# Kernel optimization log

Hardware: AMD Instinct MI355X
Metric: run time of the kernel (lower is better)

Reference implementation:

```python
import jax, jax.numpy as jnp
import numpy as np

B, L, E, H = 8, 1024, 1024, 16
D = E // H
EPS = 1e-5


def setup_inputs() -> dict:
    key = jax.random.key(0)
    ks = jax.random.split(key, 3)
    s = 1.0 / np.sqrt(E)
    return {
        "x": jax.random.normal(ks[0], (B, L, E), dtype=jnp.float32),
        "w_qkv": jax.random.normal(ks[1], (3 * E, E), dtype=jnp.float32) * s,
        "b_qkv": jnp.zeros((3 * E,), dtype=jnp.float32),
        "w_out": jax.random.normal(ks[2], (E, E), dtype=jnp.float32) * s,
        "b_out": jnp.zeros((E,), dtype=jnp.float32),
        "gamma": jnp.ones((E,), dtype=jnp.float32),
        "beta": jnp.zeros((E,), dtype=jnp.float32),
    }


def reference(x, w_qkv, b_qkv, w_out, b_out, gamma, beta):
    # Packed QKV projection (torch nn.MultiheadAttention in_proj): (B,L,3E)
    qkv = jnp.einsum("ble,fe->blf", x, w_qkv) + b_qkv
    q, k, v = jnp.split(qkv, 3, axis=-1)
    # (B,L,H,D)
    q = q.reshape(B, L, H, D) * (1.0 / np.sqrt(D))
    k = k.reshape(B, L, H, D)
    v = v.reshape(B, L, H, D)
    scores = jnp.einsum("blhd,bmhd->bhlm", q, k)           # (B,H,L,L)
    w = jax.nn.softmax(scores, axis=-1)                     # (B,H,L,L)
    ctx = jnp.einsum("bhlm,bmhd->blhd", w, v).reshape(B, L, E)
    attn_out = jnp.einsum("ble,fe->blf", ctx, w_out) + b_out
    # Residual + LayerNorm
    h = x + attn_out
    mu = h.mean(axis=-1, keepdims=True)
    var = ((h - mu) ** 2).mean(axis=-1, keepdims=True)
    hn = (h - mu) * jax.lax.rsqrt(var + EPS) * gamma + beta
    pooled = hn.mean(axis=1)                                # (B,E)
    # torch returns head-averaged weights (B,L,L); then mean over query dim
    avg_attn = w.mean(axis=1).mean(axis=1)                  # (B,L)
    return pooled, avg_attn
```

## Files before the change

### kernel.cpp

```cpp
#include <hip/hip_runtime.h>
#include <math.h>

constexpr int Bc = 8;
constexpr int Lc = 1024;
constexpr int Ec = 1024;
constexpr int Hc = 16;
constexpr int Dc = 64;
constexpr float EPSc = 1e-5f;

typedef _Float16 f16;
typedef f16 half8 __attribute__((ext_vector_type(8)));
typedef float floatx4 __attribute__((ext_vector_type(4)));

static __device__ inline void gload_lds16(const f16* g, f16* l) {
    __builtin_amdgcn_global_load_lds(
        (const __attribute__((address_space(1))) void*)g,
        (__attribute__((address_space(3))) void*)l, 16, 0, 0);
}

__global__ __launch_bounds__(256)
void cvt_f32_f16_kernel(const float* __restrict__ src, f16* __restrict__ dst, int n8) {
    int i = blockIdx.x * 256 + threadIdx.x;
    const int stride = gridDim.x * 256;
    for (; i < n8; i += stride) {
        float4 a = *(const float4*)(src + (size_t)i * 8);
        float4 b = *(const float4*)(src + (size_t)i * 8 + 4);
        half8 p;
        p[0] = (f16)a.x; p[1] = (f16)a.y; p[2] = (f16)a.z; p[3] = (f16)a.w;
        p[4] = (f16)b.x; p[5] = (f16)b.y; p[6] = (f16)b.z; p[7] = (f16)b.w;
        *(half8*)(dst + (size_t)i * 8) = p;
    }
}

__global__ __launch_bounds__(256)
void gemm_nt_h(const f16* __restrict__ A, const f16* __restrict__ Bm,
               const float* __restrict__ bias, float* __restrict__ Cf,
               f16* __restrict__ Ch, int M, int N, int K) {
    constexpr int TILE = 128;
    constexpr int KT = 32;
    __shared__ __align__(16) f16 As[TILE * KT];
    __shared__ __align__(16) f16 Bs[TILE * KT];

    const int tid = threadIdx.x;
    const int bm = blockIdx.x * TILE;
    const int bn = blockIdx.y * TILE;

    const int wave = tid >> 6;
    const int lane = tid & 63;
    const int wm = (wave >> 1) * 64;
    const int wn = (wave & 1) * 64;
    const int r16 = lane & 15;
    const int kg = lane >> 4;
    const int kswz = kg ^ ((r16 >> 1) & 3);

    floatx4 acc[4][4];
#pragma unroll
    for (int i = 0; i < 4; ++i)
#pragma unroll
        for (int j = 0; j < 4; ++j) acc[i][j] = (floatx4){0.f, 0.f, 0.f, 0.f};

    const int c0 = tid, c1 = 256 + tid;
    const int row0 = c0 >> 2, row1 = c1 >> 2;
    const int kc0 = (c0 & 3) ^ ((row0 >> 1) & 3);
    const int kc1 = (c1 & 3) ^ ((row1 >> 1) & 3);
    const f16* a0p = A + (size_t)(bm + row0) * K + kc0 * 8;
    const f16* a1p = A + (size_t)(bm + row1) * K + kc1 * 8;
    const f16* b0p = Bm + (size_t)(bn + row0) * K + kc0 * 8;
    const f16* b1p = Bm + (size_t)(bn + row1) * K + kc1 * 8;
    f16* asl0 = As + c0 * 8;
    f16* asl1 = As + c1 * 8;
    f16* bsl0 = Bs + c0 * 8;
    f16* bsl1 = Bs + c1 * 8;

    for (int k0 = 0; k0 < K; k0 += KT) {
        __syncthreads();
        gload_lds16(a0p + k0, asl0);
        gload_lds16(a1p + k0, asl1);
        gload_lds16(b0p + k0, bsl0);
        gload_lds16(b1p + k0, bsl1);
        __syncthreads();

        half8 af[4], bf[4];
#pragma unroll
        for (int i = 0; i < 4; ++i)
            af[i] = *(const half8*)&As[(wm + 16 * i + r16) * KT + kswz * 8];
#pragma unroll
        for (int j = 0; j < 4; ++j)
            bf[j] = *(const half8*)&Bs[(wn + 16 * j + r16) * KT + kswz * 8];
#pragma unroll
        for (int i = 0; i < 4; ++i)
#pragma unroll
            for (int j = 0; j < 4; ++j)
                acc[i][j] = __builtin_amdgcn_mfma_f32_16x16x32_f16(af[i], bf[j], acc[i][j], 0, 0, 0);
    }

    if (Ch) {
#pragma unroll
        for (int j = 0; j < 4; ++j) {
            const int col = bn + wn + 16 * j + r16;
            const float bv = bias[col];
#pragma unroll
            for (int i = 0; i < 4; ++i) {
                const int row0e = bm + wm + 16 * i + kg * 4;
#pragma unroll
                for (int r = 0; r < 4; ++r)
                    Ch[(size_t)(row0e + r) * N + col] = (f16)(acc[i][j][r] + bv);
            }
        }
    } else {
#pragma unroll
        for (int j = 0; j < 4; ++j) {
            const int col = bn + wn + 16 * j + r16;
            const float bv = bias[col];
#pragma unroll
            for (int i = 0; i < 4; ++i) {
                const int row0e = bm + wm + 16 * i + kg * 4;
#pragma unroll
                for (int r = 0; r < 4; ++r)
                    Cf[(size_t)(row0e + r) * N + col] = acc[i][j][r] + bv;
            }
        }
    }
}

constexpr int AQT = 128;
constexpr int AKT = 128;
constexpr int AKP = 72;
constexpr int AWP = 136;
constexpr int AVP = 136;

constexpr int AQ_OFF  = 0;
constexpr int AKV_OFF = 4608;
constexpr int AW_OFF  = AKV_OFF + 4608;
constexpr int ARS_OFF = AW_OFF + 8704;
constexpr int ACOL_OFF = ARS_OFF + 128;
constexpr int ASMEM   = ACOL_OFF + 1024;

__global__ __launch_bounds__(256, 2)
void attn_kernel(const f16* __restrict__ qkv, f16* __restrict__ ctx,
                 float* __restrict__ avg_out) {
    __shared__ __align__(16) float smemf[ASMEM];
    f16* Kq = (f16*)(smemf + AQ_OFF);
    f16* Kt = (f16*)(smemf + AKV_OFF);
    f16* Vt = (f16*)(smemf + AKV_OFF);
    f16* WS = (f16*)(smemf + AW_OFF);
    float* RS  = smemf + ARS_OFF;
    float* COL = smemf + ACOL_OFF;

    const int tid = threadIdx.x;
    const int qt = blockIdx.x, h = blockIdx.y, b = blockIdx.z;
    const int l0 = qt * AQT;
    const size_t rowstride = 3 * Ec;
    const f16* base = qkv + (size_t)b * Lc * rowstride + (size_t)h * Dc;

    const int wave = tid >> 6, lane = tid & 63;
    const int r16 = lane & 15, kg = lane >> 4;
    const int wm = (wave >> 1) * 64;
    const int wn = (wave & 1) * 64;

    if (tid < 128) RS[tid] = 0.f;
#pragma unroll
    for (int t = 0; t < 4; ++t) COL[t * 256 + tid] = 0.f;

    const int srow = tid >> 1;
    const int sh = (tid & 1) * 32;

    {
        const f16* src = base + (size_t)(l0 + srow) * rowstride + sh;
        f16* dst = Kq + srow * AKP + sh;
#pragma unroll
        for (int jj = 0; jj < 4; ++jj) {
            half8 p = *(const half8*)(src + jj * 8);
#pragma unroll
            for (int e = 0; e < 8; ++e) p[e] = p[e] * (f16)0.125f;
            *(half8*)(dst + jj * 8) = p;
        }
    }

    float rs[4][4];
#pragma unroll
    for (int i = 0; i < 4; ++i)
#pragma unroll
        for (int r = 0; r < 4; ++r) rs[i][r] = 0.f;

    for (int kt = 0; kt < Lc / AKT; ++kt) {
        __syncthreads();
        {
            const f16* src = base + (size_t)(kt * AKT + srow) * rowstride + Ec + sh;
            f16* dst = Kt + srow * AKP + sh;
#pragma unroll
            for (int jj = 0; jj < 4; ++jj)
                *(half8*)(dst + jj * 8) = *(const half8*)(src + jj * 8);
        }
        __syncthreads();

        floatx4 s[4][4];
#pragma unroll
        for (int i = 0; i < 4; ++i)
#pragma unroll
            for (int j = 0; j < 4; ++j) s[i][j] = (floatx4){0.f, 0.f, 0.f, 0.f};
#pragma unroll
        for (int ks = 0; ks < 2; ++ks) {
            half8 af[4], bf[4];
#pragma unroll
            for (int i = 0; i < 4; ++i)
                af[i] = *(const half8*)&Kq[(wm + 16 * i + r16) * AKP + ks * 32 + kg * 8];
#pragma unroll
            for (int j = 0; j < 4; ++j)
                bf[j] = *(const half8*)&Kt[(wn + 16 * j + r16) * AKP + ks * 32 + kg * 8];
#pragma unroll
            for (int i = 0; i < 4; ++i)
#pragma unroll
                for (int j = 0; j < 4; ++j)
                    s[i][j] = __builtin_amdgcn_mfma_f32_16x16x32_f16(af[i], bf[j], s[i][j], 0, 0, 0);
        }
#pragma unroll
        for (int i = 0; i < 4; ++i)
#pragma unroll
            for (int r = 0; r < 4; ++r)
                rs[i][r] += __expf(s[i][0][r]) + __expf(s[i][1][r]) +
                            __expf(s[i][2][r]) + __expf(s[i][3][r]);
    }

#pragma unroll
    for (int i = 0; i < 4; ++i)
#pragma unroll
        for (int r = 0; r < 4; ++r) {
            float v = rs[i][r];
            v += __shfl_xor(v, 1); v += __shfl_xor(v, 2);
            v += __shfl_xor(v, 4); v += __shfl_xor(v, 8);
            rs[i][r] = v;
        }
    if (r16 == 0) {
#pragma unroll
        for (int i = 0; i < 4; ++i)
#pragma unroll
            for (int r = 0; r < 4; ++r)
                atomicAdd(&RS[wm + 16 * i + 4 * kg + r], rs[i][r]);
    }
    __syncthreads();
    if (tid < 128) RS[tid] = 1.0f / RS[tid];
    __syncthreads();

    float rinv[4][4];
#pragma unroll
    for (int i = 0; i < 4; ++i)
#pragma unroll
        for (int r = 0; r < 4; ++r) rinv[i][r] = RS[wm + 16 * i + 4 * kg + r];

    floatx4 cacc[2][4];
#pragma unroll
    for (int p = 0; p < 2; ++p)
#pragma unroll
        for (int j = 0; j < 4; ++j) cacc[p][j] = (floatx4){0.f, 0.f, 0.f, 0.f};
    const int qb = wave * 32;

    for (int kt = 0; kt < Lc / AKT; ++kt) {
        __syncthreads();
        {
            const f16* src = base + (size_t)(kt * AKT + srow) * rowstride + Ec + sh;
            f16* dst = Kt + srow * AKP + sh;
#pragma unroll
            for (int jj = 0; jj < 4; ++jj)
                *(half8*)(dst + jj * 8) = *(const half8*)(src + jj * 8);
        }
        __syncthreads();

        floatx4 s[4][4];
#pragma unroll
        for (int i = 0; i < 4; ++i)
#pragma unroll
            for (int j = 0; j < 4; ++j) s[i][j] = (floatx4){0.f, 0.f, 0.f, 0.f};
#pragma unroll
        for (int ks = 0; ks < 2; ++ks) {
            half8 af[4], bf[4];
#pragma unroll
            for (int i = 0; i < 4; ++i)
                af[i] = *(const half8*)&Kq[(wm + 16 * i + r16) * AKP + ks * 32 + kg * 8];
#pragma unroll
            for (int j = 0; j < 4; ++j)
                bf[j] = *(const half8*)&Kt[(wn + 16 * j + r16) * AKP + ks * 32 + kg * 8];
#pragma unroll
            for (int i = 0; i < 4; ++i)
#pragma unroll
                for (int j = 0; j < 4; ++j)
                    s[i][j] = __builtin_amdgcn_mfma_f32_16x16x32_f16(af[i], bf[j], s[i][j], 0, 0, 0);
        }

        float cs[4] = {0.f, 0.f, 0.f, 0.f};
#pragma unroll
        for (int i = 0; i < 4; ++i)
#pragma unroll
            for (int j = 0; j < 4; ++j)
#pragma unroll
                for (int r = 0; r < 4; ++r) {
                    float w = __expf(s[i][j][r]) * rinv[i][r];
                    s[i][j][r] = w;
                    cs[j] += w;
                }

        __syncthreads();

#pragma unroll
        for (int i = 0; i < 4; ++i)
#pragma unroll
            for (int r = 0; r < 4; ++r) {
                f16* wrow = WS + (wm + 16 * i + 4 * kg + r) * AWP + wn + r16;
#pragma unroll
                for (int j = 0; j < 4; ++j) wrow[16 * j] = (f16)s[i][j][r];
            }

        {
            const f16* src = base + (size_t)(kt * AKT + srow) * rowstride + 2 * Ec + sh;
#pragma unroll
            for (int jj = 0; jj < 4; ++jj) {
                half8 v = *(const half8*)(src + jj * 8);
#pragma unroll
                for (int e = 0; e < 8; ++e)
                    Vt[(sh + jj * 8 + e) * AVP + srow] = v[e];
            }
        }

#pragma unroll
        for (int j = 0; j < 4; ++j) {
            float c = cs[j];
            c += __shfl_xor(c, 16);
            c += __shfl_xor(c, 32);
            if (kg == 0) atomicAdd(&COL[kt * AKT + wn + 16 * j + r16], c);
        }

        __syncthreads();

#pragma unroll
        for (int ks2 = 0; ks2 < 4; ++ks2) {
            half8 wa[2], vb[4];
#pragma unroll
            for (int p = 0; p < 2; ++p)
                wa[p] = *(const half8*)&WS[(qb + 16 * p + r16) * AWP + ks2 * 32 + kg * 8];
#pragma unroll
            for (int j = 0; j < 4; ++j)
                vb[j] = *(const half8*)&Vt[(16 * j + r16) * AVP + ks2 * 32 + kg * 8];
#pragma unroll
            for (int p = 0; p < 2; ++p)
#pragma unroll
                for (int j = 0; j < 4; ++j)
                    cacc[p][j] = __builtin_amdgcn_mfma_f32_16x16x32_f16(wa[p], vb[j], cacc[p][j], 0, 0, 0);
        }
    }

#pragma unroll
    for (int p = 0; p < 2; ++p)
#pragma unroll
        for (int r = 0; r < 4; ++r) {
            f16* dst = ctx + (size_t)(b * Lc + l0 + qb + 16 * p + 4 * kg + r) * Ec + h * Dc + r16;
#pragma unroll
            for (int j = 0; j < 4; ++j) dst[16 * j] = (f16)cacc[p][j][r];
        }

    __syncthreads();
#pragma unroll
    for (int t = 0; t < 4; ++t) {
        int m = t * 256 + tid;
        atomicAdd(&avg_out[b * Lc + m], COL[m] * (1.0f / (Hc * Lc)));
    }
}

__global__ __launch_bounds__(256)
void stats_kernel(const float* __restrict__ x, const float* __restrict__ attn_out,
                  float2* __restrict__ stats) {
    const int row = blockIdx.x;
    const int tid = threadIdx.x;
    const float* xp = x + (size_t)row * Ec;
    const float* ap = attn_out + (size_t)row * Ec;
    float4 xv = *(const float4*)(xp + tid * 4);
    float4 av = *(const float4*)(ap + tid * 4);
    float h0 = xv.x + av.x, h1 = xv.y + av.y, h2 = xv.z + av.z, h3 = xv.w + av.w;
    float s = h0 + h1 + h2 + h3;
    float ss = h0 * h0 + h1 * h1 + h2 * h2 + h3 * h3;
#pragma unroll
    for (int off = 32; off; off >>= 1) {
        s += __shfl_xor(s, off);
        ss += __shfl_xor(ss, off);
    }
    __shared__ float wsum[4], wsq[4];
    const int wave = tid >> 6, lane = tid & 63;
    if (lane == 0) { wsum[wave] = s; wsq[wave] = ss; }
    __syncthreads();
    if (tid == 0) {
        float ts = wsum[0] + wsum[1] + wsum[2] + wsum[3];
        float tq = wsq[0] + wsq[1] + wsq[2] + wsq[3];
        float mean = ts * (1.0f / Ec);
        float var = tq * (1.0f / Ec) - mean * mean;
        stats[row] = make_float2(mean, rsqrtf(var + EPSc));
    }
}

__global__ __launch_bounds__(256)
void pool_kernel(const float* __restrict__ x, const float* __restrict__ attn_out,
                 const float2* __restrict__ stats, const float* __restrict__ gamma,
                 const float* __restrict__ beta, float* __restrict__ pooled) {
    const int b = blockIdx.z;
    const int f = blockIdx.y * 256 + threadIdx.x;
    const int l0 = blockIdx.x * 64;
    const float g = gamma[f];
    const float be = beta[f];
    float acc = 0.f;
    for (int l = l0; l < l0 + 64; ++l) {
        size_t idx = (size_t)(b * Lc + l) * Ec + f;
        float2 st = stats[b * Lc + l];
        float h = x[idx] + attn_out[idx];
        acc += (h - st.x) * st.y * g + be;
    }
    atomicAdd(&pooled[b * Ec + f], acc * (1.0f / Lc));
}

extern "C" void kernel_launch(void* const* d_in, const int* in_sizes, int n_in,
                              void* d_out, int out_size, void* d_ws, size_t ws_size,
                              hipStream_t stream) {
    const float* x      = (const float*)d_in[0];
    const float* w_qkv  = (const float*)d_in[1];
    const float* b_qkv  = (const float*)d_in[2];
    const float* w_out  = (const float*)d_in[3];
    const float* b_out  = (const float*)d_in[4];
    const float* gamma  = (const float*)d_in[5];
    const float* beta   = (const float*)d_in[6];
    float* out = (float*)d_out;

    f16* wsh = (f16*)d_ws;
    f16* qkv_h  = wsh;
    f16* ctx_h  = qkv_h + (size_t)25165824;
    f16* x_h    = ctx_h + (size_t)8388608;
    f16* wqkv_h = x_h + (size_t)8388608;
    f16* wout_h = wqkv_h + (size_t)3145728;
    float* attn_out = (float*)(wout_h + (size_t)1048576);
    float* stats = attn_out + (size_t)8388608;

    const int M = Bc * Lc;

    hipMemsetAsync(d_out, 0, (size_t)out_size * sizeof(float), stream);

    cvt_f32_f16_kernel<<<2048, 256, 0, stream>>>(x, x_h, (Bc * Lc * Ec) / 8);
    cvt_f32_f16_kernel<<<1536, 256, 0, stream>>>(w_qkv, wqkv_h, (3 * Ec * Ec) / 8);
    cvt_f32_f16_kernel<<<512, 256, 0, stream>>>(w_out, wout_h, (Ec * Ec) / 8);

    dim3 g1(M / 128, (3 * Ec) / 128);
    gemm_nt_h<<<g1, 256, 0, stream>>>(x_h, wqkv_h, b_qkv, nullptr, qkv_h, M, 3 * Ec, Ec);

    dim3 g2(Lc / AQT, Hc, Bc);
    attn_kernel<<<g2, 256, 0, stream>>>(qkv_h, ctx_h, out + Bc * Ec);

    dim3 g3(M / 128, Ec / 128);
    gemm_nt_h<<<g3, 256, 0, stream>>>(ctx_h, wout_h, b_out, attn_out, nullptr, M, Ec, Ec);

    stats_kernel<<<M, 256, 0, stream>>>(x, attn_out, (float2*)stats);

    dim3 g5(16, 4, Bc);
    pool_kernel<<<g5, 256, 0, stream>>>(x, attn_out, (float2*)stats, gamma, beta, out);
}
```

Measured before the change: 342.1 us.

## Hold Q in registers per wave and shrink key tiles to raise occupancy

```diff
diff --git a/kernel.cpp b/kernel.cpp
--- a/kernel.cpp
+++ b/kernel.cpp
@@ -124,27 +124,24 @@
 }
 
 constexpr int AQT = 128;
-constexpr int AKT = 128;
-constexpr int AKP = 72;
-constexpr int AWP = 136;
-constexpr int AVP = 136;
-
-constexpr int AQ_OFF  = 0;
-constexpr int AKV_OFF = 4608;
-constexpr int AW_OFF  = AKV_OFF + 4608;
-constexpr int ARS_OFF = AW_OFF + 8704;
-constexpr int ACOL_OFF = ARS_OFF + 128;
+constexpr int AKT = 64;
+constexpr int NKT = Lc / AKT;
+constexpr int AKP = 68;
+constexpr int AVP = 72;
+constexpr int AWP = 68;
+
+constexpr int AKV_OFF = 0;
+constexpr int AW_OFF  = 2304;
+constexpr int ACOL_OFF = AW_OFF + 4352;
 constexpr int ASMEM   = ACOL_OFF + 1024;
 
-__global__ __launch_bounds__(256, 2)
+__global__ __launch_bounds__(256, 4)
 void attn_kernel(const f16* __restrict__ qkv, f16* __restrict__ ctx,
                  float* __restrict__ avg_out) {
     __shared__ __align__(16) float smemf[ASMEM];
-    f16* Kq = (f16*)(smemf + AQ_OFF);
     f16* Kt = (f16*)(smemf + AKV_OFF);
     f16* Vt = (f16*)(smemf + AKV_OFF);
     f16* WS = (f16*)(smemf + AW_OFF);
-    float* RS  = smemf + ARS_OFF;
     float* COL = smemf + ACOL_OFF;
 
     const int tid = threadIdx.x;
@@ -155,141 +152,115 @@
 
     const int wave = tid >> 6, lane = tid & 63;
     const int r16 = lane & 15, kg = lane >> 4;
-    const int wm = (wave >> 1) * 64;
-    const int wn = (wave & 1) * 64;
-
-    if (tid < 128) RS[tid] = 0.f;
+    const int qw = wave * 32;
+
 #pragma unroll
     for (int t = 0; t < 4; ++t) COL[t * 256 + tid] = 0.f;
 
-    const int srow = tid >> 1;
-    const int sh = (tid & 1) * 32;
-
-    {
-        const f16* src = base + (size_t)(l0 + srow) * rowstride + sh;
-        f16* dst = Kq + srow * AKP + sh;
-#pragma unroll
-        for (int jj = 0; jj < 4; ++jj) {
-            half8 p = *(const half8*)(src + jj * 8);
+    const int sk = tid & 63;
+    const int sd = (tid >> 6) * 16;
+
+    half8 qf[2][2];
+#pragma unroll
+    for (int i = 0; i < 2; ++i)
+#pragma unroll
+        for (int ks = 0; ks < 2; ++ks) {
+            const f16* src = base + (size_t)(l0 + qw + 16 * i + r16) * rowstride + ks * 32 + kg * 8;
+            half8 p = *(const half8*)src;
 #pragma unroll
             for (int e = 0; e < 8; ++e) p[e] = p[e] * (f16)0.125f;
-            *(half8*)(dst + jj * 8) = p;
-        }
-    }
-
-    float rs[4][4];
-#pragma unroll
-    for (int i = 0; i < 4; ++i)
+            qf[i][ks] = p;
+        }
+
+    float rs[2][4];
+#pragma unroll
+    for (int i = 0; i < 2; ++i)
 #pragma unroll
         for (int r = 0; r < 4; ++r) rs[i][r] = 0.f;
 
-    for (int kt = 0; kt < Lc / AKT; ++kt) {
+    for (int kt = 0; kt < NKT; ++kt) {
         __syncthreads();
         {
-            const f16* src = base + (size_t)(kt * AKT + srow) * rowstride + Ec + sh;
-            f16* dst = Kt + srow * AKP + sh;
-#pragma unroll
-            for (int jj = 0; jj < 4; ++jj)
-                *(half8*)(dst + jj * 8) = *(const half8*)(src + jj * 8);
-        }
-        __syncthreads();
-
-        floatx4 s[4][4];
-#pragma unroll
-        for (int i = 0; i < 4; ++i)
+            const f16* src = base + (size_t)(kt * AKT + sk) * rowstride + Ec + sd;
+            f16* dst = Kt + sk * AKP + sd;
+            *(half8*)(dst)     = *(const half8*)(src);
+            *(half8*)(dst + 8) = *(const half8*)(src + 8);
+        }
+        __syncthreads();
+
+        floatx4 s[2][4];
+#pragma unroll
+        for (int i = 0; i < 2; ++i)
 #pragma unroll
             for (int j = 0; j < 4; ++j) s[i][j] = (floatx4){0.f, 0.f, 0.f, 0.f};
 #pragma unroll
         for (int ks = 0; ks < 2; ++ks) {
-            half8 af[4], bf[4];
-#pragma unroll
-            for (int i = 0; i < 4; ++i)
-                af[i] = *(const half8*)&Kq[(wm + 16 * i + r16) * AKP + ks * 32 + kg * 8];
+            half8 bf[4];
 #pragma unroll
             for (int j = 0; j < 4; ++j)
-                bf[j] = *(const half8*)&Kt[(wn + 16 * j + r16) * AKP + ks * 32 + kg * 8];
-#pragma unroll
-            for (int i = 0; i < 4; ++i)
+                bf[j] = *(const half8*)&Kt[(16 * j + r16) * AKP + ks * 32 + kg * 8];
+#pragma unroll
+            for (int i = 0; i < 2; ++i)
 #pragma unroll
                 for (int j = 0; j < 4; ++j)
-                    s[i][j] = __builtin_amdgcn_mfma_f32_16x16x32_f16(af[i], bf[j], s[i][j], 0, 0, 0);
-        }
-#pragma unroll
-        for (int i = 0; i < 4; ++i)
+                    s[i][j] = __builtin_amdgcn_mfma_f32_16x16x32_f16(qf[i][ks], bf[j], s[i][j], 0, 0, 0);
+        }
+#pragma unroll
+        for (int i = 0; i < 2; ++i)
 #pragma unroll
             for (int r = 0; r < 4; ++r)
                 rs[i][r] += __expf(s[i][0][r]) + __expf(s[i][1][r]) +
                             __expf(s[i][2][r]) + __expf(s[i][3][r]);
     }
 
-#pragma unroll
-    for (int i = 0; i < 4; ++i)
+    float rinv[2][4];
+#pragma unroll
+    for (int i = 0; i < 2; ++i)
 #pragma unroll
         for (int r = 0; r < 4; ++r) {
             float v = rs[i][r];
             v += __shfl_xor(v, 1); v += __shfl_xor(v, 2);
             v += __shfl_xor(v, 4); v += __shfl_xor(v, 8);
-            rs[i][r] = v;
-        }
-    if (r16 == 0) {
-#pragma unroll
-        for (int i = 0; i < 4; ++i)
-#pragma unroll
-            for (int r = 0; r < 4; ++r)
-                atomicAdd(&RS[wm + 16 * i + 4 * kg + r], rs[i][r]);
-    }
-    __syncthreads();
-    if (tid < 128) RS[tid] = 1.0f / RS[tid];
-    __syncthreads();
-
-    float rinv[4][4];
-#pragma unroll
-    for (int i = 0; i < 4; ++i)
-#pragma unroll
-        for (int r = 0; r < 4; ++r) rinv[i][r] = RS[wm + 16 * i + 4 * kg + r];
+            rinv[i][r] = 1.0f / v;
+        }
 
     floatx4 cacc[2][4];
 #pragma unroll
     for (int p = 0; p < 2; ++p)
 #pragma unroll
         for (int j = 0; j < 4; ++j) cacc[p][j] = (floatx4){0.f, 0.f, 0.f, 0.f};
-    const int qb = wave * 32;
-
-    for (int kt = 0; kt < Lc / AKT; ++kt) {
+
+    for (int kt = 0; kt < NKT; ++kt) {
         __syncthreads();
         {
-            const f16* src = base + (size_t)(kt * AKT + srow) * rowstride + Ec + sh;
-            f16* dst = Kt + srow * AKP + sh;
-#pragma unroll
-            for (int jj = 0; jj < 4; ++jj)
-                *(half8*)(dst + jj * 8) = *(const half8*)(src + jj * 8);
-        }
-        __syncthreads();
-
-        floatx4 s[4][4];
-#pragma unroll
-        for (int i = 0; i < 4; ++i)
+            const f16* src = base + (size_t)(kt * AKT + sk) * rowstride + Ec + sd;
+            f16* dst = Kt + sk * AKP + sd;
+            *(half8*)(dst)     = *(const half8*)(src);
+            *(half8*)(dst + 8) = *(const half8*)(src + 8);
+        }
+        __syncthreads();
+
+        floatx4 s[2][4];
+#pragma unroll
+        for (int i = 0; i < 2; ++i)
 #pragma unroll
             for (int j = 0; j < 4; ++j) s[i][j] = (floatx4){0.f, 0.f, 0.f, 0.f};
 #pragma unroll
         for (int ks = 0; ks < 2; ++ks) {
-            half8 af[4], bf[4];
-#pragma unroll
-            for (int i = 0; i < 4; ++i)
-                af[i] = *(const half8*)&Kq[(wm + 16 * i + r16) * AKP + ks * 32 + kg * 8];
+            half8 bf[4];
 #pragma unroll
             for (int j = 0; j < 4; ++j)
-                bf[j] = *(const half8*)&Kt[(wn + 16 * j + r16) * AKP + ks * 32 + kg * 8];
-#pragma unroll
-            for (int i = 0; i < 4; ++i)
+                bf[j] = *(const half8*)&Kt[(16 * j + r16) * AKP + ks * 32 + kg * 8];
+#pragma unroll
+            for (int i = 0; i < 2; ++i)
 #pragma unroll
                 for (int j = 0; j < 4; ++j)
-                    s[i][j] = __builtin_amdgcn_mfma_f32_16x16x32_f16(af[i], bf[j], s[i][j], 0, 0, 0);
+                    s[i][j] = __builtin_amdgcn_mfma_f32_16x16x32_f16(qf[i][ks], bf[j], s[i][j], 0, 0, 0);
         }
 
         float cs[4] = {0.f, 0.f, 0.f, 0.f};
 #pragma unroll
-        for (int i = 0; i < 4; ++i)
+        for (int i = 0; i < 2; ++i)
 #pragma unroll
             for (int j = 0; j < 4; ++j)
 #pragma unroll
@@ -302,22 +273,22 @@
         __syncthreads();
 
 #pragma unroll
-        for (int i = 0; i < 4; ++i)
+        for (int i = 0; i < 2; ++i)
 #pragma unroll
             for (int r = 0; r < 4; ++r) {
-                f16* wrow = WS + (wm + 16 * i + 4 * kg + r) * AWP + wn + r16;
+                f16* wrow = WS + (qw + 16 * i + 4 * kg + r) * AWP + r16;
 #pragma unroll
                 for (int j = 0; j < 4; ++j) wrow[16 * j] = (f16)s[i][j][r];
             }
 
         {
-            const f16* src = base + (size_t)(kt * AKT + srow) * rowstride + 2 * Ec + sh;
-#pragma unroll
-            for (int jj = 0; jj < 4; ++jj) {
-                half8 v = *(const half8*)(src + jj * 8);
-#pragma unroll
-                for (int e = 0; e < 8; ++e)
-                    Vt[(sh + jj * 8 + e) * AVP + srow] = v[e];
+            const f16* src = base + (size_t)(kt * AKT + sk) * rowstride + 2 * Ec + sd;
+            half8 v0 = *(const half8*)(src);
+            half8 v1 = *(const half8*)(src + 8);
+#pragma unroll
+            for (int e = 0; e < 8; ++e) {
+                Vt[(sd + e) * AVP + sk]     = v0[e];
+                Vt[(sd + 8 + e) * AVP + sk] = v1[e];
             }
         }
 
@@ -326,17 +297,17 @@
             float c = cs[j];
             c += __shfl_xor(c, 16);
             c += __shfl_xor(c, 32);
-            if (kg == 0) atomicAdd(&COL[kt * AKT + wn + 16 * j + r16], c);
-        }
-
-        __syncthreads();
-
-#pragma unroll
-        for (int ks2 = 0; ks2 < 4; ++ks2) {
+            if (kg == 0) atomicAdd(&COL[kt * AKT + 16 * j + r16], c);
+        }
+
+        __syncthreads();
+
+#pragma unroll
+        for (int ks2 = 0; ks2 < 2; ++ks2) {
             half8 wa[2], vb[4];
 #pragma unroll
             for (int p = 0; p < 2; ++p)
-                wa[p] = *(const half8*)&WS[(qb + 16 * p + r16) * AWP + ks2 * 32 + kg * 8];
+                wa[p] = *(const half8*)&WS[(qw + 16 * p + r16) * AWP + ks2 * 32 + kg * 8];
 #pragma unroll
             for (int j = 0; j < 4; ++j)
                 vb[j] = *(const half8*)&Vt[(16 * j + r16) * AVP + ks2 * 32 + kg * 8];
@@ -352,7 +323,7 @@
     for (int p = 0; p < 2; ++p)
 #pragma unroll
         for (int r = 0; r < 4; ++r) {
-            f16* dst = ctx + (size_t)(b * Lc + l0 + qb + 16 * p + 4 * kg + r) * Ec + h * Dc + r16;
+            f16* dst = ctx + (size_t)(b * Lc + l0 + qw + 16 * p + 4 * kg + r) * Ec + h * Dc + r16;
 #pragma unroll
             for (int j = 0; j < 4; ++j) dst[16 * j] = (f16)cacc[p][j][r];
         }
```

New measurement: 466.6 us. 1.36x slower.

## Fuse LayerNorm stats and pooling into a single-pass kernel

Applied to the files above, without the earlier changes.

```diff
diff --git a/kernel.cpp b/kernel.cpp
--- a/kernel.cpp
+++ b/kernel.cpp
@@ -366,52 +366,56 @@
 }
 
 __global__ __launch_bounds__(256)
-void stats_kernel(const float* __restrict__ x, const float* __restrict__ attn_out,
-                  float2* __restrict__ stats) {
-    const int row = blockIdx.x;
+void ln_pool_kernel(const float* __restrict__ x, const float* __restrict__ attn_out,
+                    const float* __restrict__ gamma, const float* __restrict__ beta,
+                    float* __restrict__ pooled) {
+    constexpr int RPB = 8;
+    const int b = blockIdx.y;
+    const int l0 = blockIdx.x * RPB;
     const int tid = threadIdx.x;
-    const float* xp = x + (size_t)row * Ec;
-    const float* ap = attn_out + (size_t)row * Ec;
-    float4 xv = *(const float4*)(xp + tid * 4);
-    float4 av = *(const float4*)(ap + tid * 4);
-    float h0 = xv.x + av.x, h1 = xv.y + av.y, h2 = xv.z + av.z, h3 = xv.w + av.w;
-    float s = h0 + h1 + h2 + h3;
-    float ss = h0 * h0 + h1 * h1 + h2 * h2 + h3 * h3;
-#pragma unroll
-    for (int off = 32; off; off >>= 1) {
-        s += __shfl_xor(s, off);
-        ss += __shfl_xor(ss, off);
-    }
-    __shared__ float wsum[4], wsq[4];
     const int wave = tid >> 6, lane = tid & 63;
-    if (lane == 0) { wsum[wave] = s; wsq[wave] = ss; }
-    __syncthreads();
-    if (tid == 0) {
-        float ts = wsum[0] + wsum[1] + wsum[2] + wsum[3];
-        float tq = wsq[0] + wsq[1] + wsq[2] + wsq[3];
+    __shared__ float wsum[2][4], wsq[2][4];
+
+    float acc0 = 0.f, acc1 = 0.f, acc2 = 0.f, acc3 = 0.f;
+
+    for (int r = 0; r < RPB; ++r) {
+        const size_t row = (size_t)(b * Lc + l0 + r) * Ec + tid * 4;
+        float4 xv = *(const float4*)(x + row);
+        float4 av = *(const float4*)(attn_out + row);
+        float h0 = xv.x + av.x, h1 = xv.y + av.y, h2 = xv.z + av.z, h3 = xv.w + av.w;
+        float s = h0 + h1 + h2 + h3;
+        float ss = h0 * h0 + h1 * h1 + h2 * h2 + h3 * h3;
+#pragma unroll
+        for (int off = 32; off; off >>= 1) {
+            s += __shfl_xor(s, off);
+            ss += __shfl_xor(ss, off);
+        }
+        const int p = r & 1;
+        if (lane == 0) { wsum[p][wave] = s; wsq[p][wave] = ss; }
+        __syncthreads();
+        float ts = wsum[p][0] + wsum[p][1] + wsum[p][2] + wsum[p][3];
+        float tq = wsq[p][0] + wsq[p][1] + wsq[p][2] + wsq[p][3];
         float mean = ts * (1.0f / Ec);
-        float var = tq * (1.0f / Ec) - mean * mean;
-        stats[row] = make_float2(mean, rsqrtf(var + EPSc));
-    }
-}
-
-__global__ __launch_bounds__(256)
-void pool_kernel(const float* __restrict__ x, const float* __restrict__ attn_out,
-                 const float2* __restrict__ stats, const float* __restrict__ gamma,
-                 const float* __restrict__ beta, float* __restrict__ pooled) {
-    const int b = blockIdx.z;
-    const int f = blockIdx.y * 256 + threadIdx.x;
-    const int l0 = blockIdx.x * 64;
-    const float g = gamma[f];
-    const float be = beta[f];
-    float acc = 0.f;
-    for (int l = l0; l < l0 + 64; ++l) {
-        size_t idx = (size_t)(b * Lc + l) * Ec + f;
-        float2 st = stats[b * Lc + l];
-        float h = x[idx] + attn_out[idx];
-        acc += (h - st.x) * st.y * g + be;
-    }
-    atomicAdd(&pooled[b * Ec + f], acc * (1.0f / Lc));
+        float rstd = rsqrtf(tq * (1.0f / Ec) - mean * mean + EPSc);
+        acc0 += (h0 - mean) * rstd;
+        acc1 += (h1 - mean) * rstd;
+        acc2 += (h2 - mean) * rstd;
+        acc3 += (h3 - mean) * rstd;
+    }
+
+    const int f = tid * 4;
+    float4 g = *(const float4*)(gamma + f);
+    float4 be = *(const float4*)(beta + f);
+    float r0 = acc0 * g.x * (1.0f / Lc);
+    float r1 = acc1 * g.y * (1.0f / Lc);
+    float r2 = acc2 * g.z * (1.0f / Lc);
+    float r3 = acc3 * g.w * (1.0f / Lc);
+    if (blockIdx.x == 0) { r0 += be.x; r1 += be.y; r2 += be.z; r3 += be.w; }
+    float* dst = pooled + (size_t)b * Ec + f;
+    atomicAdd(dst + 0, r0);
+    atomicAdd(dst + 1, r1);
+    atomicAdd(dst + 2, r2);
+    atomicAdd(dst + 3, r3);
 }
 
 extern "C" void kernel_launch(void* const* d_in, const int* in_sizes, int n_in,
@@ -433,7 +437,6 @@
     f16* wqkv_h = x_h + (size_t)8388608;
     f16* wout_h = wqkv_h + (size_t)3145728;
     float* attn_out = (float*)(wout_h + (size_t)1048576);
-    float* stats = attn_out + (size_t)8388608;
 
     const int M = Bc * Lc;
 
@@ -452,8 +455,6 @@
     dim3 g3(M / 128, Ec / 128);
     gemm_nt_h<<<g3, 256, 0, stream>>>(ctx_h, wout_h, b_out, attn_out, nullptr, M, Ec, Ec);
 
-    stats_kernel<<<M, 256, 0, stream>>>(x, attn_out, (float2*)stats);
-
-    dim3 g5(16, 4, Bc);
-    pool_kernel<<<g5, 256, 0, stream>>>(x, attn_out, (float2*)stats, gamma, beta, out);
-}
+    dim3 g4(Lc / 8, Bc);
+    ln_pool_kernel<<<g4, 256, 0, stream>>>(x, attn_out, gamma, beta, out);
+}
```

New measurement: 357.3 us. +4.5%, slower.

## Double GEMM K-tile to 64 and store LDS tiles k-chunk-major

Applied to the files above, without the earlier changes.

```diff
diff --git a/kernel.cpp b/kernel.cpp
--- a/kernel.cpp
+++ b/kernel.cpp
@@ -37,7 +37,7 @@
                const float* __restrict__ bias, float* __restrict__ Cf,
                f16* __restrict__ Ch, int M, int N, int K) {
     constexpr int TILE = 128;
-    constexpr int KT = 32;
+    constexpr int KT = 64;
     __shared__ __align__(16) f16 As[TILE * KT];
     __shared__ __align__(16) f16 Bs[TILE * KT];
 
@@ -51,7 +51,6 @@
     const int wn = (wave & 1) * 64;
     const int r16 = lane & 15;
     const int kg = lane >> 4;
-    const int kswz = kg ^ ((r16 >> 1) & 3);
 
     floatx4 acc[4][4];
 #pragma unroll
@@ -59,39 +58,38 @@
 #pragma unroll
         for (int j = 0; j < 4; ++j) acc[i][j] = (floatx4){0.f, 0.f, 0.f, 0.f};
 
-    const int c0 = tid, c1 = 256 + tid;
-    const int row0 = c0 >> 2, row1 = c1 >> 2;
-    const int kc0 = (c0 & 3) ^ ((row0 >> 1) & 3);
-    const int kc1 = (c1 & 3) ^ ((row1 >> 1) & 3);
-    const f16* a0p = A + (size_t)(bm + row0) * K + kc0 * 8;
-    const f16* a1p = A + (size_t)(bm + row1) * K + kc1 * 8;
-    const f16* b0p = Bm + (size_t)(bn + row0) * K + kc0 * 8;
-    const f16* b1p = Bm + (size_t)(bn + row1) * K + kc1 * 8;
-    f16* asl0 = As + c0 * 8;
-    f16* asl1 = As + c1 * 8;
-    f16* bsl0 = Bs + c0 * 8;
-    f16* bsl1 = Bs + c1 * 8;
+    const int srow = tid & 127;
+    const int kcb = tid >> 7;
+    const f16* ap = A + (size_t)(bm + srow) * K;
+    const f16* bp = Bm + (size_t)(bn + srow) * K;
+    f16* asl = As + tid * 8;
+    f16* bsl = Bs + tid * 8;
 
     for (int k0 = 0; k0 < K; k0 += KT) {
         __syncthreads();
-        gload_lds16(a0p + k0, asl0);
-        gload_lds16(a1p + k0, asl1);
-        gload_lds16(b0p + k0, bsl0);
-        gload_lds16(b1p + k0, bsl1);
-        __syncthreads();
-
-        half8 af[4], bf[4];
-#pragma unroll
-        for (int i = 0; i < 4; ++i)
-            af[i] = *(const half8*)&As[(wm + 16 * i + r16) * KT + kswz * 8];
-#pragma unroll
-        for (int j = 0; j < 4; ++j)
-            bf[j] = *(const half8*)&Bs[(wn + 16 * j + r16) * KT + kswz * 8];
-#pragma unroll
-        for (int i = 0; i < 4; ++i)
+#pragma unroll
+        for (int q = 0; q < 4; ++q) {
+            const int kc = kcb + 2 * q;
+            gload_lds16(ap + k0 + kc * 8, asl + q * 2048);
+            gload_lds16(bp + k0 + kc * 8, bsl + q * 2048);
+        }
+        __syncthreads();
+
+#pragma unroll
+        for (int ks = 0; ks < 2; ++ks) {
+            half8 af[4], bf[4];
+#pragma unroll
+            for (int i = 0; i < 4; ++i)
+                af[i] = *(const half8*)&As[((ks * 4 + kg) * 128 + wm + 16 * i + r16) * 8];
 #pragma unroll
             for (int j = 0; j < 4; ++j)
-                acc[i][j] = __builtin_amdgcn_mfma_f32_16x16x32_f16(af[i], bf[j], acc[i][j], 0, 0, 0);
+                bf[j] = *(const half8*)&Bs[((ks * 4 + kg) * 128 + wn + 16 * j + r16) * 8];
+#pragma unroll
+            for (int i = 0; i < 4; ++i)
+#pragma unroll
+                for (int j = 0; j < 4; ++j)
+                    acc[i][j] = __builtin_amdgcn_mfma_f32_16x16x32_f16(af[i], bf[j], acc[i][j], 0, 0, 0);
+        }
     }
 
     if (Ch) {
```

Measured after the change: 388.2 us. +13.5%, slower.
